# Optimization experiments

Hardware: AMD Instinct MI355X
Metric: run time of the kernel (lower is better)

Reference implementation:

```python
import jax, jax.numpy as jnp
import numpy as np

N = 1681  # 41*41, fixed by the /1681 normalization in the original loss
BS = 32

def setup_inputs() -> dict:
    key = jax.random.key(0)
    k1, k2 = jax.random.split(key)
    pred = jax.random.normal(k1, (BS, N, N), dtype=jnp.float32)
    target = jax.random.normal(k2, (BS, N, N), dtype=jnp.float32)
    return {"pred": pred, "target": target}

def _col_scale_by_row_norm(x):
    # no = 1/sqrt(sum_k x[l, j, k]^2)  -> per-row L2 norm reciprocal, shape [bs, N]
    # x @ diag(no) scales COLUMN j by no[j]; replace O(N^2 D) matmul with
    inv_rn = 1.0 / jnp.sqrt(jnp.sum(x * x, axis=2))  # [bs, N]
    return x * inv_rn[:, None, :]

def reference(pred, target):
    bs = pred.shape[0]
    p = _col_scale_by_row_norm(pred)
    t = _col_scale_by_row_norm(target)
    losses = -jnp.sum(p * t, axis=(1, 2))  # [bs]
    return jnp.sum(losses) / bs / 1681.0
```

## Files before the change

### kernel.cpp

```cpp
#include <hip/hip_runtime.h>

#define N 1681
#define BS 32
#define BAND 41
#define NBLOCKS (BS * BAND)
#define THREADS 256
#define NROWS_TOTAL (BS * N)
#define MAXC ((BS * N * N) / 4)


__global__ __launch_bounds__(THREADS, 2) void pass1_kernel(
    const float* __restrict__ pred,
    const float* __restrict__ targ,
    float* __restrict__ sp,
    float* __restrict__ st,
    float* __restrict__ dpart) {
  __shared__ float dsum[N];

  const int b    = blockIdx.x;
  const int tid  = threadIdx.x;
  const int lane = tid & 63;
  const int wid  = tid >> 6;
  const long R0  = (long)b * BAND;

  for (int idx = tid; idx < N; idx += THREADS) dsum[idx] = 0.0f;
  __syncthreads();

  const float4* __restrict__ pred4 = (const float4*)pred;
  const float4* __restrict__ targ4 = (const float4*)targ;

  const int h = wid;
  float dprod[7][4];
#pragma unroll
  for (int t2 = 0; t2 < 7; ++t2)
#pragma unroll
    for (int ee = 0; ee < 4; ++ee) dprod[t2][ee] = 0.0f;

  float4 pA[7], tA[7], pB[7], tB[7];

#define LOADROW(PBUF, TBUF, CBASE) do {                                  \
    _Pragma("unroll")                                                    \
    for (int t2 = 0; t2 < 7; ++t2) {                                     \
      const int c_ = min((CBASE) + t2 * 64 + lane, MAXC - 1);            \
      PBUF[t2] = pred4[c_];                                              \
      TBUF[t2] = targ4[c_];                                              \
    }                                                                    \
  } while (0)

#define COMPROW(PBUF, TBUF, RR) do {                                     \
    const long R_ = R0 + (RR);                                           \
    float psq = 0.0f, tsq = 0.0f;                                        \
    _Pragma("unroll")                                                    \
    for (int t2 = 0; t2 < 7; ++t2) {                                     \
      const float pv[4] = {PBUF[t2].x, PBUF[t2].y, PBUF[t2].z, PBUF[t2].w}; \
      const float tv[4] = {TBUF[t2].x, TBUF[t2].y, TBUF[t2].z, TBUF[t2].w}; \
      if (t2 == 0 || t2 == 6) {                                          \
        const int colb = t2 * 256 + 4 * lane - h;                        \
        _Pragma("unroll")                                                \
        for (int ee = 0; ee < 4; ++ee) {                                 \
          const bool ok = (unsigned)(colb + ee) < (unsigned)N;           \
          const float pm = ok ? pv[ee] : 0.0f;                           \
          const float tm = ok ? tv[ee] : 0.0f;                           \
          psq = fmaf(pm, pm, psq);                                       \
          tsq = fmaf(tm, tm, tsq);                                       \
          dprod[t2][ee] = fmaf(pm, tm, dprod[t2][ee]);                   \
        }                                                                \
      } else {                                                           \
        _Pragma("unroll")                                                \
        for (int ee = 0; ee < 4; ++ee) {                                 \
          psq = fmaf(pv[ee], pv[ee], psq);                               \
          tsq = fmaf(tv[ee], tv[ee], tsq);                               \
          dprod[t2][ee] = fmaf(pv[ee], tv[ee], dprod[t2][ee]);           \
        }                                                                \
      }                                                                  \
    }                                                                    \
    _Pragma("unroll")                                                    \
    for (int off = 32; off > 0; off >>= 1) {                             \
      psq += __shfl_down(psq, off, 64);                                  \
      tsq += __shfl_down(tsq, off, 64);                                  \
    }                                                                    \
    if (lane == 0) { sp[R_] = psq; st[R_] = tsq; }                       \
  } while (0)

  const int rr0 = (wid - (int)(R0 & 3)) & 3;
  const int c0  = (int)(((R0 + rr0) * (long)N) >> 2);

  int rr = rr0;
  int cA = c0;
  LOADROW(pA, tA, cA);
  for (;;) {
    const int r1 = rr + 4;
    if (r1 < BAND) LOADROW(pB, tB, cA + N);
    COMPROW(pA, tA, rr);
    if (r1 >= BAND) break;
    const int r2 = r1 + 4;
    if (r2 < BAND) LOADROW(pA, tA, cA + 2 * N);
    COMPROW(pB, tB, r1);
    if (r2 >= BAND) break;
    rr = r2;
    cA += 2 * N;
  }

#pragma unroll
  for (int t2 = 0; t2 < 7; ++t2)
#pragma unroll
    for (int ee = 0; ee < 4; ++ee) {
      const int col = t2 * 256 + 4 * lane + ee - h;
      if ((unsigned)col < (unsigned)N) atomicAdd(&dsum[col], dprod[t2][ee]);
    }
  __syncthreads();

  for (int idx = tid; idx < N; idx += THREADS)
    dpart[(size_t)b * N + idx] = dsum[idx];
}

__global__ __launch_bounds__(THREADS) void fin1_kernel(
    const float* __restrict__ sp,
    const float* __restrict__ st,
    const float* __restrict__ dpart,
    double* __restrict__ bsums) {
  __shared__ double red[4];

  double acc = 0.0;
  for (int g = blockIdx.x * THREADS + threadIdx.x; g < NROWS_TOTAL;
       g += gridDim.x * THREADS) {
    const int l = g / N;
    const int j = g - l * N;
    float dv = 0.0f;
    const float* __restrict__ dp = dpart + (size_t)l * BAND * N + j;
#pragma unroll 41
    for (int band = 0; band < BAND; ++band) dv += dp[(size_t)band * N];
    const double s = (double)sp[g] * (double)st[g];
    acc += (double)dv / sqrt(s);
  }
#pragma unroll
  for (int off = 32; off > 0; off >>= 1) acc += __shfl_down(acc, off, 64);
  const int wid = threadIdx.x >> 6;
  if ((threadIdx.x & 63) == 0) red[wid] = acc;
  __syncthreads();
  if (threadIdx.x == 0)
    bsums[blockIdx.x] = red[0] + red[1] + red[2] + red[3];
}

__global__ __launch_bounds__(64) void fin2_kernel(
    const double* __restrict__ bsums, float* __restrict__ out) {
  double acc = bsums[threadIdx.x] + bsums[threadIdx.x + 64];
#pragma unroll
  for (int off = 32; off > 0; off >>= 1) acc += __shfl_down(acc, off, 64);
  if (threadIdx.x == 0)
    out[0] = (float)(-acc / ((double)BS * (double)N));
}

extern "C" void kernel_launch(void* const* d_in, const int* in_sizes, int n_in,
                              void* d_out, int out_size, void* d_ws, size_t ws_size,
                              hipStream_t stream) {
  const float* pred = (const float*)d_in[0];
  const float* targ = (const float*)d_in[1];

  float* ws     = (float*)d_ws;
  float* dpart  = ws;
  float* sp     = ws + (size_t)NBLOCKS * N;
  float* st     = sp + (size_t)NROWS_TOTAL;
  double* bsums = (double*)(st + (size_t)NROWS_TOTAL + 32);

  pass1_kernel<<<NBLOCKS, THREADS, 0, stream>>>(pred, targ, sp, st, dpart);
  fin1_kernel<<<128, THREADS, 0, stream>>>(sp, st, dpart, bsums);
  fin2_kernel<<<1, 64, 0, stream>>>(bsums, (float*)d_out);
}
```

Baseline: 164.2 us.

## Stream rows through LDS with async global_load_lds double buffering and split bands

Replaces the register double-buffered row loads with asynchronous global-to-LDS copies (global_load_lds), double-buffered per wave and synchronized with explicit vmcnt waits. Each 41-row band is split across two blocks, doubling the grid and the number of partial column-sum rows that fin1 must reduce. Per-row norms are staged in shared memory and written out at the end. The intent is more bytes in flight and lower VGPR pressure; the cost is more partial-sum traffic and reliance on hand-counted vmcnt values being correct.

```diff
diff --git a/kernel.cpp b/kernel.cpp
--- a/kernel.cpp
+++ b/kernel.cpp
@@ -2,60 +2,74 @@
 
 #define N 1681
 #define BS 32
-#define BAND 41
-#define NBLOCKS (BS * BAND)
 #define THREADS 256
 #define NROWS_TOTAL (BS * N)
 #define MAXC ((BS * N * N) / 4)
+#define NBLK (BS * 41 * 2)
+#define PARTS_PER_MAT 82
 
 
-__global__ __launch_bounds__(THREADS, 2) void pass1_kernel(
+typedef __attribute__((address_space(1))) const void* gas_ptr;
+typedef __attribute__((address_space(3))) void* las_ptr;
+
+__device__ __forceinline__ void async16(const float4* g, const float4* l) {
+  __builtin_amdgcn_global_load_lds((gas_ptr)g, (las_ptr)l, 16, 0, 0);
+}
+
+union SM {
+  float4 stage[4][2][2][448];
+  float dsum[N];
+};
+
+__global__ __launch_bounds__(THREADS) void pass1_kernel(
     const float* __restrict__ pred,
     const float* __restrict__ targ,
     float* __restrict__ sp,
     float* __restrict__ st,
     float* __restrict__ dpart) {
-  __shared__ float dsum[N];
+  __shared__ SM sm;
+  __shared__ float spl[21], stl[21];
 
   const int b    = blockIdx.x;
   const int tid  = threadIdx.x;
   const int lane = tid & 63;
   const int wid  = tid >> 6;
-  const long R0  = (long)b * BAND;
-
-  for (int idx = tid; idx < N; idx += THREADS) dsum[idx] = 0.0f;
-  __syncthreads();
+  const int band = b >> 1;
+  const int halfsel = b & 1;
+  const int Rbase = band * 41 + halfsel * 21;
+  const int nr    = halfsel ? 20 : 21;
+  const int h     = wid;
+  const int rr0   = (h - (Rbase & 3)) & 3;
+  const int nrw   = (nr - rr0 + 3) >> 2;
 
   const float4* __restrict__ pred4 = (const float4*)pred;
   const float4* __restrict__ targ4 = (const float4*)targ;
 
-  const int h = wid;
   float dprod[7][4];
 #pragma unroll
   for (int t2 = 0; t2 < 7; ++t2)
 #pragma unroll
     for (int ee = 0; ee < 4; ++ee) dprod[t2][ee] = 0.0f;
 
-  float4 pA[7], tA[7], pB[7], tB[7];
-
-#define LOADROW(PBUF, TBUF, CBASE) do {                                  \
+#define ISSUE(BUF, Q) do {                                               \
     _Pragma("unroll")                                                    \
-    for (int t2 = 0; t2 < 7; ++t2) {                                     \
-      const int c_ = min((CBASE) + t2 * 64 + lane, MAXC - 1);            \
-      PBUF[t2] = pred4[c_];                                              \
-      TBUF[t2] = targ4[c_];                                              \
+    for (int t2_ = 0; t2_ < 7; ++t2_) {                                  \
+      const int c_ = min((Q) + t2_ * 64 + lane, MAXC - 1);               \
+      async16(pred4 + c_, &sm.stage[wid][BUF][0][t2_ * 64]);             \
+      async16(targ4 + c_, &sm.stage[wid][BUF][1][t2_ * 64]);             \
     }                                                                    \
   } while (0)
 
-#define COMPROW(PBUF, TBUF, RR) do {                                     \
-    const long R_ = R0 + (RR);                                           \
+#define COMPUTE(BUF, RIDX) do {                                          \
     float psq = 0.0f, tsq = 0.0f;                                        \
     _Pragma("unroll")                                                    \
-    for (int t2 = 0; t2 < 7; ++t2) {                                     \
-      const float pv[4] = {PBUF[t2].x, PBUF[t2].y, PBUF[t2].z, PBUF[t2].w}; \
-      const float tv[4] = {TBUF[t2].x, TBUF[t2].y, TBUF[t2].z, TBUF[t2].w}; \
-      if (t2 == 0 || t2 == 6) {                                          \
-        const int colb = t2 * 256 + 4 * lane - h;                        \
+    for (int t2_ = 0; t2_ < 7; ++t2_) {                                  \
+      const float4 p4 = sm.stage[wid][BUF][0][t2_ * 64 + lane];          \
+      const float4 t4 = sm.stage[wid][BUF][1][t2_ * 64 + lane];          \
+      const float pv[4] = {p4.x, p4.y, p4.z, p4.w};                      \
+      const float tv[4] = {t4.x, t4.y, t4.z, t4.w};                      \
+      if (t2_ == 0 || t2_ == 6) {                                        \
+        const int colb = t2_ * 256 + 4 * lane - h;                       \
         _Pragma("unroll")                                                \
         for (int ee = 0; ee < 4; ++ee) {                                 \
           const bool ok = (unsigned)(colb + ee) < (unsigned)N;           \
@@ -63,14 +77,14 @@
           const float tm = ok ? tv[ee] : 0.0f;                           \
           psq = fmaf(pm, pm, psq);                                       \
           tsq = fmaf(tm, tm, tsq);                                       \
-          dprod[t2][ee] = fmaf(pm, tm, dprod[t2][ee]);                   \
+          dprod[t2_][ee] = fmaf(pm, tm, dprod[t2_][ee]);                 \
         }                                                                \
       } else {                                                           \
         _Pragma("unroll")                                                \
         for (int ee = 0; ee < 4; ++ee) {                                 \
           psq = fmaf(pv[ee], pv[ee], psq);                               \
           tsq = fmaf(tv[ee], tv[ee], tsq);                               \
-          dprod[t2][ee] = fmaf(pv[ee], tv[ee], dprod[t2][ee]);           \
+          dprod[t2_][ee] = fmaf(pv[ee], tv[ee], dprod[t2_][ee]);         \
         }                                                                \
       }                                                                  \
     }                                                                    \
@@ -79,39 +93,43 @@
       psq += __shfl_down(psq, off, 64);                                  \
       tsq += __shfl_down(tsq, off, 64);                                  \
     }                                                                    \
-    if (lane == 0) { sp[R_] = psq; st[R_] = tsq; }                       \
+    if (lane == 0) { spl[RIDX] = psq; stl[RIDX] = tsq; }                 \
   } while (0)
 
-  const int rr0 = (wid - (int)(R0 & 3)) & 3;
-  const int c0  = (int)(((R0 + rr0) * (long)N) >> 2);
-
-  int rr = rr0;
-  int cA = c0;
-  LOADROW(pA, tA, cA);
-  for (;;) {
-    const int r1 = rr + 4;
-    if (r1 < BAND) LOADROW(pB, tB, cA + N);
-    COMPROW(pA, tA, rr);
-    if (r1 >= BAND) break;
-    const int r2 = r1 + 4;
-    if (r2 < BAND) LOADROW(pA, tA, cA + 2 * N);
-    COMPROW(pB, tB, r1);
-    if (r2 >= BAND) break;
-    rr = r2;
-    cA += 2 * N;
+  int R   = Rbase + rr0;
+  int q   = (R * N) >> 2;
+  int rem = nrw;
+  int buf = 0;
+  ISSUE(0, q);
+  while (rem > 0) {
+    const bool more = (rem > 1);
+    if (more) {
+      ISSUE(buf ^ 1, q + 1681);
+      asm volatile("s_waitcnt vmcnt(14)" ::: "memory");
+    } else {
+      asm volatile("s_waitcnt vmcnt(0)" ::: "memory");
+    }
+    COMPUTE(buf, R - Rbase);
+    buf ^= 1; R += 4; q += 1681; --rem;
   }
 
+  __syncthreads();
+  for (int idx = tid; idx < N; idx += THREADS) sm.dsum[idx] = 0.0f;
+  __syncthreads();
 #pragma unroll
   for (int t2 = 0; t2 < 7; ++t2)
 #pragma unroll
     for (int ee = 0; ee < 4; ++ee) {
       const int col = t2 * 256 + 4 * lane + ee - h;
-      if ((unsigned)col < (unsigned)N) atomicAdd(&dsum[col], dprod[t2][ee]);
+      if ((unsigned)col < (unsigned)N) atomicAdd(&sm.dsum[col], dprod[t2][ee]);
     }
   __syncthreads();
-
   for (int idx = tid; idx < N; idx += THREADS)
-    dpart[(size_t)b * N + idx] = dsum[idx];
+    dpart[(size_t)b * N + idx] = sm.dsum[idx];
+  if (tid < nr) {
+    sp[Rbase + tid] = spl[tid];
+    st[Rbase + tid] = stl[tid];
+  }
 }
 
 __global__ __launch_bounds__(THREADS) void fin1_kernel(
@@ -126,10 +144,9 @@
        g += gridDim.x * THREADS) {
     const int l = g / N;
     const int j = g - l * N;
+    const float* __restrict__ dp = dpart + (size_t)l * PARTS_PER_MAT * N + j;
     float dv = 0.0f;
-    const float* __restrict__ dp = dpart + (size_t)l * BAND * N + j;
-#pragma unroll 41
-    for (int band = 0; band < BAND; ++band) dv += dp[(size_t)band * N];
+    for (int p = 0; p < PARTS_PER_MAT; ++p) dv += dp[(size_t)p * N];
     const double s = (double)sp[g] * (double)st[g];
     acc += (double)dv / sqrt(s);
   }
@@ -157,13 +174,12 @@
   const float* pred = (const float*)d_in[0];
   const float* targ = (const float*)d_in[1];
 
-  float* ws     = (float*)d_ws;
-  float* dpart  = ws;
-  float* sp     = ws + (size_t)NBLOCKS * N;
-  float* st     = sp + (size_t)NROWS_TOTAL;
-  double* bsums = (double*)(st + (size_t)NROWS_TOTAL + 32);
+  double* bsums = (double*)d_ws;
+  float*  dpart = (float*)(bsums + 128);
+  float*  sp    = dpart + (size_t)NBLK * N;
+  float*  st    = sp + (size_t)NROWS_TOTAL;
 
-  pass1_kernel<<<NBLOCKS, THREADS, 0, stream>>>(pred, targ, sp, st, dpart);
+  pass1_kernel<<<NBLK, THREADS, 0, stream>>>(pred, targ, sp, st, dpart);
   fin1_kernel<<<128, THREADS, 0, stream>>>(sp, st, dpart, bsums);
   fin2_kernel<<<1, 64, 0, stream>>>(bsums, (float*)d_out);
 }
```

Measured after the change: 278.4 us. 69.5% more time.
